# Kernel tuning notes

Measured on AMD Instinct MI355X. Metric: run time of the kernel, lower is better.

## Reference

```python
import jax, jax.numpy as jnp
import numpy as np

N_SRC = 50000
N_DST = 50000
N_EDGES = 800000
D_IN = 256
NUM_HEADS = 8
OUT_DIM = 16
NEG_SLOPE = 0.2


def setup_inputs() -> dict:
    key = jax.random.key(0)
    ks = jax.random.split(key, 9)
    feat_src = jax.random.normal(ks[0], (N_SRC, D_IN), dtype=jnp.float32)
    feat_dst = jax.random.normal(ks[1], (N_DST, D_IN), dtype=jnp.float32)
    W_src = jax.random.normal(ks[2], (NUM_HEADS * OUT_DIM, D_IN), dtype=jnp.float32) * 0.05
    b_src = jax.random.normal(ks[3], (NUM_HEADS * OUT_DIM,), dtype=jnp.float32) * 0.05
    W_dst = jax.random.normal(ks[4], (NUM_HEADS * OUT_DIM, D_IN), dtype=jnp.float32) * 0.05
    b_dst = jax.random.normal(ks[5], (NUM_HEADS * OUT_DIM,), dtype=jnp.float32) * 0.05
    attn = jax.random.normal(ks[6], (NUM_HEADS, 2 * OUT_DIM), dtype=jnp.float32) * 0.1
    src_idx = jax.random.randint(ks[7], (N_EDGES,), 0, N_SRC, dtype=jnp.int32)
    dst_idx = jax.random.randint(ks[8], (N_EDGES,), 0, N_DST, dtype=jnp.int32)
    return {"feat_src": feat_src, "feat_dst": feat_dst, "W_src": W_src,
            "b_src": b_src, "W_dst": W_dst, "b_dst": b_dst, "attn": attn,
            "src_idx": src_idx, "dst_idx": dst_idx}


def reference(feat_src, feat_dst, W_src, b_src, W_dst, b_dst, attn, src_idx, dst_idx):
    # Node-type-specific linear transforms (feat_drop=0 at inference)
    hs = (feat_src @ W_src.T + b_src).reshape(N_SRC, NUM_HEADS, OUT_DIM)
    hd = (feat_dst @ W_dst.T + b_dst).reshape(N_DST, NUM_HEADS, OUT_DIM)
    # Per-node attention logits: el_i = <hs_i, a_l>, er_j = <hd_j, a_r>
    el = jnp.einsum('nkd,kd->nk', hs, attn[:, :OUT_DIM])  # (N_src, K)
    er = jnp.einsum('nkd,kd->nk', hd, attn[:, OUT_DIM:])  # (N_dst, K)
    # Edge scores: e_uv = LeakyReLU(el_u + er_v)
    e = el[src_idx] + er[dst_idx]                          # (E, K)
    e = jnp.where(e >= 0, e, NEG_SLOPE * e)
    # Edge softmax over incoming edges of each destination node
    m = jax.ops.segment_max(e, dst_idx, num_segments=N_DST)        # (N_dst, K)
    e_exp = jnp.exp(e - m[dst_idx])
    denom = jax.ops.segment_sum(e_exp, dst_idx, num_segments=N_DST)
    a = e_exp / denom[dst_idx]                             # (E, K)
    # Weighted neighbor aggregation: sum_u a_uv * hs_u
    msg = hs[src_idx] * a[:, :, None]                      # (E, K, d_out)
    out = jax.ops.segment_sum(msg, dst_idx, num_segments=N_DST)
    return out.reshape(N_DST, NUM_HEADS * OUT_DIM)
```

## Files before the change

### kernel.cpp

```cpp
#include <hip/hip_runtime.h>
#include <hip/hip_bf16.h>

#define N_SRCC 50000
#define N_DSTC 50000
#define N_EDG 800000
#define NBUK 500
#define DPB 100
#define BCAP 2048
#define EPB 3334
#define NPB 240
#define GEMB 391

typedef __attribute__((ext_vector_type(8))) short bf16x8;
typedef __attribute__((ext_vector_type(4))) float f32x4;
typedef __attribute__((ext_vector_type(8))) unsigned short us8;

__device__ inline short f2bf(float x) {
  __hip_bfloat16 b = __float2bfloat16(x);
  return *reinterpret_cast<short*>(&b);
}
__device__ inline float bf2f(unsigned hi16) {
  union { unsigned u; float f; } c; c.u = hi16 << 16; return c.f;
}

__global__ void fold_kernel(const float* __restrict__ Wsrc, const float* __restrict__ bsrc,
                            const float* __restrict__ Wdst, const float* __restrict__ bdst,
                            const float* __restrict__ attn,
                            float* __restrict__ U, float* __restrict__ Cc,
                            short* __restrict__ Wbf, short* __restrict__ Ubf,
                            int* __restrict__ bCur) {
  int t = blockIdx.x * blockDim.x + threadIdx.x;
  if (t < 4096) {
    int side = t >> 11;
    int r = (t >> 8) & 7;
    int c = t & 255;
    const float* W = side ? Wdst : Wsrc;
    float s = 0.f;
    #pragma unroll
    for (int d = 0; d < 16; d++)
      s += attn[r*32 + side*16 + d] * W[(r*16 + d)*256 + c];
    U[t] = s;
    if (side == 1) Ubf[r*256 + c] = f2bf(s);
    else           Ubf[2048 + t]  = 0;
    const float4* p = (const float4*)&Wsrc[t*8];
    float4 v0 = p[0], v1 = p[1];
    bf16x8 w;
    w[0]=f2bf(v0.x); w[1]=f2bf(v0.y); w[2]=f2bf(v0.z); w[3]=f2bf(v0.w);
    w[4]=f2bf(v1.x); w[5]=f2bf(v1.y); w[6]=f2bf(v1.z); w[7]=f2bf(v1.w);
    *(bf16x8*)&Wbf[t*8] = w;
  }
  if (t < 16) {
    int side = t >> 3, r = t & 7;
    const float* b = side ? bdst : bsrc;
    float s = 0.f;
    #pragma unroll
    for (int d = 0; d < 16; d++) s += attn[r*32 + side*16 + d] * b[r*16 + d];
    Cc[t] = s;
  }
  if (t < NBUK) bCur[t] = 0;
}

__global__ __launch_bounds__(256) void mega(
    const float* __restrict__ feat_src, const float* __restrict__ feat_dst,
    const short* __restrict__ Wbf, const short* __restrict__ Ubf,
    const float* __restrict__ bias, const float* __restrict__ attn,
    const float* __restrict__ Cc,
    const int* __restrict__ src, const int* __restrict__ dst,
    int* __restrict__ bCur, unsigned* __restrict__ bData,
    __hip_bfloat16* __restrict__ hsC, float* __restrict__ el,
    float* __restrict__ er) {
  __shared__ __align__(16) char smem[20480];
  int b = blockIdx.x;
  int t = threadIdx.x;

  if (b < NPB) {
    int* h   = (int*)smem;
    int* cur = (int*)(smem + 2048);
    for (int i = t; i < NBUK; i += 256) h[i] = 0;
    __syncthreads();
    int start = b * EPB;
    int end = min(start + EPB, N_EDG);
    for (int e = start + t; e < end; e += 256)
      atomicAdd(&h[dst[e] / DPB], 1);
    __syncthreads();
    for (int i = t; i < NBUK; i += 256) {
      int c = h[i];
      cur[i] = c ? atomicAdd(&bCur[i], c) : 0;
    }
    __syncthreads();
    for (int e = start + t; e < end; e += 256) {
      int d = dst[e], bk = d / DPB;
      int pos = atomicAdd(&cur[bk], 1);
      if (pos < BCAP)
        bData[(size_t)bk*BCAP + pos] = (unsigned)src[e] | ((unsigned)(d - bk*DPB) << 16);
    }
    return;
  }

  if (b < NPB + GEMB) {
    short (*As)[40] = (short(*)[40])smem;
    short (*Bs)[40] = (short(*)[40])(smem + 10240);
    int lane = t & 63, wid = t >> 6;
    int wr = wid >> 1, wc = wid & 1;
    int row0 = (b - NPB) * 128;
    int lr = lane & 15, lk = lane >> 4;
    int sr = t >> 1, skq = (t & 1) * 16;
    f32x4 acc[4][4] = {};
    for (int k0 = 0; k0 < 256; k0 += 32) {
      {
        int gr = row0 + sr;
        float4 v0 = {}, v1 = {}, v2 = {}, v3 = {};
        if (gr < N_SRCC) {
          const float4* p = (const float4*)&feat_src[(size_t)gr*256 + k0 + skq];
          v0 = p[0]; v1 = p[1]; v2 = p[2]; v3 = p[3];
        }
        bf16x8 t0, t1;
        t0[0]=f2bf(v0.x); t0[1]=f2bf(v0.y); t0[2]=f2bf(v0.z); t0[3]=f2bf(v0.w);
        t0[4]=f2bf(v1.x); t0[5]=f2bf(v1.y); t0[6]=f2bf(v1.z); t0[7]=f2bf(v1.w);
        t1[0]=f2bf(v2.x); t1[1]=f2bf(v2.y); t1[2]=f2bf(v2.z); t1[3]=f2bf(v2.w);
        t1[4]=f2bf(v3.x); t1[5]=f2bf(v3.y); t1[6]=f2bf(v3.z); t1[7]=f2bf(v3.w);
        *(bf16x8*)&As[sr][skq]     = t0;
        *(bf16x8*)&As[sr][skq + 8] = t1;
      }
      *(bf16x8*)&Bs[sr][skq]     = *(const bf16x8*)&Wbf[sr*256 + k0 + skq];
      *(bf16x8*)&Bs[sr][skq + 8] = *(const bf16x8*)&Wbf[sr*256 + k0 + skq + 8];
      __syncthreads();
      bf16x8 af[4], bfr[4];
      #pragma unroll
      for (int m = 0; m < 4; m++)
        af[m] = *(const bf16x8*)&As[wr*64 + m*16 + lr][lk*8];
      #pragma unroll
      for (int n = 0; n < 4; n++)
        bfr[n] = *(const bf16x8*)&Bs[wc*64 + n*16 + lr][lk*8];
      #pragma unroll
      for (int m = 0; m < 4; m++)
        #pragma unroll
        for (int n = 0; n < 4; n++)
          acc[m][n] = __builtin_amdgcn_mfma_f32_16x16x32_bf16(af[m], bfr[n], acc[m][n], 0, 0, 0);
      __syncthreads();
    }
    #pragma unroll
    for (int m = 0; m < 4; m++) {
      int r0 = row0 + wr*64 + m*16 + lk*4;
      #pragma unroll
      for (int n = 0; n < 4; n++) {
        int col = wc*64 + n*16 + lr;
        int h = wc*4 + n;
        float bv = bias[col];
        float al = attn[h*32 + lr];
        #pragma unroll
        for (int j = 0; j < 4; j++) {
          int gr = r0 + j;
          float hv = acc[m][n][j] + bv;
          if (gr < N_SRCC) hsC[(size_t)gr*128 + col] = __float2bfloat16(hv);
          float p = hv * al;
          p += __shfl_xor(p, 1); p += __shfl_xor(p, 2);
          p += __shfl_xor(p, 4); p += __shfl_xor(p, 8);
          if (lr == 0 && gr < N_SRCC) el[gr*8 + h] = p;
        }
      }
    }
    return;
  }

  {
    short (*As)[40]  = (short(*)[40])smem;
    short (*Bu)[264] = (short(*)[264])(smem + 10240);
    int lane = t & 63, wid = t >> 6;
    int row0 = (b - NPB - GEMB) * 128;
    int lr = lane & 15, lk = lane >> 4;
    int sr = t >> 1, skq = (t & 1) * 16;
    #pragma unroll
    for (int i = 0; i < 2; i++) {
      int c = t + i*256;
      int r = c >> 5, ck = c & 31;
      *(bf16x8*)&Bu[r][ck*8] = *(const bf16x8*)&Ubf[r*256 + ck*8];
    }
    f32x4 acc[2] = {};
    for (int k0 = 0; k0 < 256; k0 += 32) {
      {
        int gr = row0 + sr;
        float4 v0 = {}, v1 = {}, v2 = {}, v3 = {};
        if (gr < N_DSTC) {
          const float4* p = (const float4*)&feat_dst[(size_t)gr*256 + k0 + skq];
          v0 = p[0]; v1 = p[1]; v2 = p[2]; v3 = p[3];
        }
        bf16x8 t0, t1;
        t0[0]=f2bf(v0.x); t0[1]=f2bf(v0.y); t0[2]=f2bf(v0.z); t0[3]=f2bf(v0.w);
        t0[4]=f2bf(v1.x); t0[5]=f2bf(v1.y); t0[6]=f2bf(v1.z); t0[7]=f2bf(v1.w);
        t1[0]=f2bf(v2.x); t1[1]=f2bf(v2.y); t1[2]=f2bf(v2.z); t1[3]=f2bf(v2.w);
        t1[4]=f2bf(v3.x); t1[5]=f2bf(v3.y); t1[6]=f2bf(v3.z); t1[7]=f2bf(v3.w);
        *(bf16x8*)&As[sr][skq]     = t0;
        *(bf16x8*)&As[sr][skq + 8] = t1;
      }
      __syncthreads();
      bf16x8 bu = *(const bf16x8*)&Bu[lr][k0 + lk*8];
      #pragma unroll
      for (int m = 0; m < 2; m++) {
        bf16x8 af = *(const bf16x8*)&As[wid*32 + m*16 + lr][lk*8];
        acc[m] = __builtin_amdgcn_mfma_f32_16x16x32_bf16(af, bu, acc[m], 0, 0, 0);
      }
      __syncthreads();
    }
    if (lr < 8) {
      float cb = Cc[8 + lr];
      #pragma unroll
      for (int m = 0; m < 2; m++) {
        int r0 = row0 + wid*32 + m*16 + lk*4;
        #pragma unroll
        for (int j = 0; j < 4; j++) {
          int gr = r0 + j;
          if (gr < N_DSTC) er[gr*8 + lr] = acc[m][j] + cb;
        }
      }
    }
  }
}

__global__ __launch_bounds__(256) void sort_bucket(const unsigned* __restrict__ bData,
    const int* __restrict__ bCur, int* __restrict__ offS, int* __restrict__ offE,
    unsigned short* __restrict__ srcS) {
  __shared__ int hist[DPB];
  __shared__ int s[128];
  __shared__ int cur[DPB];
  int b = blockIdx.x, t = threadIdx.x;
  int cnt = min(bCur[b], BCAP);
  int base = b * BCAP;
  for (int i = t; i < DPB; i += 256) hist[i] = 0;
  __syncthreads();
  for (int e = t; e < cnt; e += 256) atomicAdd(&hist[bData[base + e] >> 16], 1);
  __syncthreads();
  if (t < 128) s[t] = (t < DPB) ? hist[t] : 0;
  __syncthreads();
  for (int d = 1; d < 128; d <<= 1) {
    int v = (t < 128 && t >= d) ? s[t - d] : 0;
    __syncthreads();
    if (t < 128) s[t] += v;
    __syncthreads();
  }
  if (t < DPB) {
    int excl = s[t] - hist[t];
    cur[t] = excl;
    offS[b * DPB + t] = base + excl;
    offE[b * DPB + t] = base + excl + hist[t];
  }
  __syncthreads();
  for (int e = t; e < cnt; e += 256) {
    unsigned ent = bData[base + e];
    int pos = atomicAdd(&cur[ent >> 16], 1);
    srcS[base + pos] = (unsigned short)(ent & 0xffffu);
  }
}

__global__ __launch_bounds__(256) void aggregate(
    const __hip_bfloat16* __restrict__ hs, const float* __restrict__ el,
    const float* __restrict__ er, const int* __restrict__ offS,
    const int* __restrict__ offE, const unsigned short* __restrict__ srcS,
    float* __restrict__ out) {
  int w = threadIdx.x >> 6;
  int lane = threadIdx.x & 63;
  int jA = blockIdx.x * 8 + w;
  int jB = jA + 4;
  int g = lane >> 4;
  int q = lane & 15;
  int h = q >> 1;
  int e0a = offS[jA], remA = offE[jA] - e0a;
  int e0b = offS[jB], remB = offE[jB] - e0b;
  float erA = er[jA*8 + h];
  float erB = er[jB*8 + h];
  float accA[8] = {}, accB[8] = {};
  float denA = 0.f, denB = 0.f;

  #define AGG_BODY(E, ERH, ACC, DEN) { \
    int s = srcS[E]; \
    float ev = el[s*8 + h] + ERH; \
    ev = ev >= 0.f ? ev : 0.2f * ev; \
    float wg = __expf(ev); \
    DEN += wg; \
    us8 hv = *(const us8*)&hs[(size_t)s*128 + q*8]; \
    _Pragma("unroll") \
    for (int c = 0; c < 8; c++) { \
      ACC[c] = fmaf(wg, bf2f((unsigned)hv[c]), ACC[c]); \
    } \
  }

  int ka = 0, kb = 0;
  while (ka + 8 <= remA && kb + 8 <= remB) {
    AGG_BODY(e0a + ka + g, erA, accA, denA);
    AGG_BODY(e0b + kb + g, erB, accB, denB);
    AGG_BODY(e0a + ka + 4 + g, erA, accA, denA);
    AGG_BODY(e0b + kb + 4 + g, erB, accB, denB);
    ka += 8; kb += 8;
  }
  while (ka + 4 <= remA && kb + 4 <= remB) {
    AGG_BODY(e0a + ka + g, erA, accA, denA);
    AGG_BODY(e0b + kb + g, erB, accB, denB);
    ka += 4; kb += 4;
  }
  while (ka + 4 <= remA) { AGG_BODY(e0a + ka + g, erA, accA, denA); ka += 4; }
  while (kb + 4 <= remB) { AGG_BODY(e0b + kb + g, erB, accB, denB); kb += 4; }
  if (ka + g < remA) AGG_BODY(e0a + ka + g, erA, accA, denA);
  if (kb + g < remB) AGG_BODY(e0b + kb + g, erB, accB, denB);
  #undef AGG_BODY

  #pragma unroll
  for (int c = 0; c < 8; c++) {
    accA[c] += __shfl_xor(accA[c], 16); accA[c] += __shfl_xor(accA[c], 32);
    accB[c] += __shfl_xor(accB[c], 16); accB[c] += __shfl_xor(accB[c], 32);
  }
  denA += __shfl_xor(denA, 16); denA += __shfl_xor(denA, 32);
  denB += __shfl_xor(denB, 16); denB += __shfl_xor(denB, 32);
  if (g == 0) {
    float invA = (remA > 0) ? 1.f / denA : 0.f;
    float invB = (remB > 0) ? 1.f / denB : 0.f;
    float4 r0, r1;
    r0.x = accA[0]*invA; r0.y = accA[1]*invA; r0.z = accA[2]*invA; r0.w = accA[3]*invA;
    r1.x = accA[4]*invA; r1.y = accA[5]*invA; r1.z = accA[6]*invA; r1.w = accA[7]*invA;
    *(float4*)&out[(size_t)jA*128 + q*8]     = r0;
    *(float4*)&out[(size_t)jA*128 + q*8 + 4] = r1;
    r0.x = accB[0]*invB; r0.y = accB[1]*invB; r0.z = accB[2]*invB; r0.w = accB[3]*invB;
    r1.x = accB[4]*invB; r1.y = accB[5]*invB; r1.z = accB[6]*invB; r1.w = accB[7]*invB;
    *(float4*)&out[(size_t)jB*128 + q*8]     = r0;
    *(float4*)&out[(size_t)jB*128 + q*8 + 4] = r1;
  }
}

extern "C" void kernel_launch(void* const* d_in, const int* in_sizes, int n_in,
                              void* d_out, int out_size, void* d_ws, size_t ws_size,
                              hipStream_t stream) {
  const float* feat_src = (const float*)d_in[0];
  const float* feat_dst = (const float*)d_in[1];
  const float* W_src = (const float*)d_in[2];
  const float* b_src = (const float*)d_in[3];
  const float* W_dst = (const float*)d_in[4];
  const float* b_dst = (const float*)d_in[5];
  const float* attn  = (const float*)d_in[6];
  const int* src_idx = (const int*)d_in[7];
  const int* dst_idx = (const int*)d_in[8];
  float* out = (float*)d_out;

  __hip_bfloat16* hs_bf = (__hip_bfloat16*)d_ws;
  float* el = (float*)(hs_bf + (size_t)N_SRCC*128);
  float* er = el + (size_t)N_SRCC*8;
  float* U  = er + (size_t)N_DSTC*8;
  float* Cc = U + 4096;
  short* Wbf = (short*)(Cc + 16);
  short* Ubf = Wbf + 32768;
  int* bCur  = (int*)(Ubf + 4096);
  int* offS  = bCur + NBUK;
  int* offE  = offS + N_DSTC;
  unsigned* bData = (unsigned*)(offE + N_DSTC);
  unsigned short* srcS = (unsigned short*)(bData + (size_t)NBUK*BCAP);

  fold_kernel<<<16, 256, 0, stream>>>(W_src, b_src, W_dst, b_dst, attn, U, Cc, Wbf, Ubf, bCur);
  mega<<<NPB + 2*GEMB, 256, 0, stream>>>(feat_src, feat_dst, Wbf, Ubf, b_src, attn,
                                         Cc, src_idx, dst_idx, bCur, bData,
                                         hs_bf, el, er);
  sort_bucket<<<NBUK, 256, 0, stream>>>(bData, bCur, offS, offE, srcS);
  aggregate<<<(N_DSTC + 7)/8, 256, 0, stream>>>(hs_bf, el, er, offS, offE, srcS, out);
}
```

Baseline: 86.60 us.

## Widen fused mega kernel to 512 threads with 256-row GEMM tiles

```diff
diff --git a/kernel.cpp b/kernel.cpp
--- a/kernel.cpp
+++ b/kernel.cpp
@@ -9,7 +9,8 @@
 #define BCAP 2048
 #define EPB 3334
 #define NPB 240
-#define GEMB 391
+#define HSB 196
+#define ERB 196
 
 typedef __attribute__((ext_vector_type(8))) short bf16x8;
 typedef __attribute__((ext_vector_type(4))) float f32x4;
@@ -60,7 +61,7 @@
   if (t < NBUK) bCur[t] = 0;
 }
 
-__global__ __launch_bounds__(256) void mega(
+__global__ __launch_bounds__(512) void mega512(
     const float* __restrict__ feat_src, const float* __restrict__ feat_dst,
     const short* __restrict__ Wbf, const short* __restrict__ Ubf,
     const float* __restrict__ bias, const float* __restrict__ attn,
@@ -69,26 +70,26 @@
     int* __restrict__ bCur, unsigned* __restrict__ bData,
     __hip_bfloat16* __restrict__ hsC, float* __restrict__ el,
     float* __restrict__ er) {
-  __shared__ __align__(16) char smem[20480];
+  __shared__ __align__(16) char smem[30720];
   int b = blockIdx.x;
   int t = threadIdx.x;
 
   if (b < NPB) {
     int* h   = (int*)smem;
     int* cur = (int*)(smem + 2048);
-    for (int i = t; i < NBUK; i += 256) h[i] = 0;
+    for (int i = t; i < NBUK; i += 512) h[i] = 0;
     __syncthreads();
     int start = b * EPB;
     int end = min(start + EPB, N_EDG);
-    for (int e = start + t; e < end; e += 256)
+    for (int e = start + t; e < end; e += 512)
       atomicAdd(&h[dst[e] / DPB], 1);
     __syncthreads();
-    for (int i = t; i < NBUK; i += 256) {
+    for (int i = t; i < NBUK; i += 512) {
       int c = h[i];
       cur[i] = c ? atomicAdd(&bCur[i], c) : 0;
     }
     __syncthreads();
-    for (int e = start + t; e < end; e += 256) {
+    for (int e = start + t; e < end; e += 512) {
       int d = dst[e], bk = d / DPB;
       int pos = atomicAdd(&cur[bk], 1);
       if (pos < BCAP)
@@ -97,15 +98,17 @@
     return;
   }
 
-  if (b < NPB + GEMB) {
+  if (b < NPB + HSB) {
     short (*As)[40] = (short(*)[40])smem;
-    short (*Bs)[40] = (short(*)[40])(smem + 10240);
+    short (*Bs)[40] = (short(*)[40])(smem + 20480);
     int lane = t & 63, wid = t >> 6;
     int wr = wid >> 1, wc = wid & 1;
-    int row0 = (b - NPB) * 128;
+    int row0 = (b - NPB) * 256;
     int lr = lane & 15, lk = lane >> 4;
     int sr = t >> 1, skq = (t & 1) * 16;
+    int br = t >> 2, bq = (t & 3) * 8;
     f32x4 acc[4][4] = {};
+
     for (int k0 = 0; k0 < 256; k0 += 32) {
       {
         int gr = row0 + sr;
@@ -122,8 +125,7 @@
         *(bf16x8*)&As[sr][skq]     = t0;
         *(bf16x8*)&As[sr][skq + 8] = t1;
       }
-      *(bf16x8*)&Bs[sr][skq]     = *(const bf16x8*)&Wbf[sr*256 + k0 + skq];
-      *(bf16x8*)&Bs[sr][skq + 8] = *(const bf16x8*)&Wbf[sr*256 + k0 + skq + 8];
+      *(bf16x8*)&Bs[br][bq] = *(const bf16x8*)&Wbf[br*256 + k0 + bq];
       __syncthreads();
       bf16x8 af[4], bfr[4];
       #pragma unroll
@@ -165,15 +167,13 @@
 
   {
     short (*As)[40]  = (short(*)[40])smem;
-    short (*Bu)[264] = (short(*)[264])(smem + 10240);
-    int lane = t & 63, wid = t >> 6;
-    int row0 = (b - NPB - GEMB) * 128;
+    short (*Bu)[264] = (short(*)[264])(smem + 20480);
+    int lane = t & 63, w = t >> 6;
+    int row0 = (b - NPB - HSB) * 256;
     int lr = lane & 15, lk = lane >> 4;
     int sr = t >> 1, skq = (t & 1) * 16;
-    #pragma unroll
-    for (int i = 0; i < 2; i++) {
-      int c = t + i*256;
-      int r = c >> 5, ck = c & 31;
+    {
+      int r = t >> 5, ck = t & 31;
       *(bf16x8*)&Bu[r][ck*8] = *(const bf16x8*)&Ubf[r*256 + ck*8];
     }
     f32x4 acc[2] = {};
@@ -197,7 +197,7 @@
       bf16x8 bu = *(const bf16x8*)&Bu[lr][k0 + lk*8];
       #pragma unroll
       for (int m = 0; m < 2; m++) {
-        bf16x8 af = *(const bf16x8*)&As[wid*32 + m*16 + lr][lk*8];
+        bf16x8 af = *(const bf16x8*)&As[w*32 + m*16 + lr][lk*8];
         acc[m] = __builtin_amdgcn_mfma_f32_16x16x32_bf16(af, bu, acc[m], 0, 0, 0);
       }
       __syncthreads();
@@ -206,11 +206,11 @@
       float cb = Cc[8 + lr];
       #pragma unroll
       for (int m = 0; m < 2; m++) {
-        int r0 = row0 + wid*32 + m*16 + lk*4;
+        int r0 = row0 + w*32 + m*16 + lk*4;
         #pragma unroll
         for (int j = 0; j < 4; j++) {
-          int gr = r0 + j;
-          if (gr < N_DSTC) er[gr*8 + lr] = acc[m][j] + cb;
+          int gr2 = r0 + j;
+          if (gr2 < N_DSTC) er[gr2*8 + lr] = acc[m][j] + cb;
         }
       }
     }
@@ -353,9 +353,9 @@
   unsigned short* srcS = (unsigned short*)(bData + (size_t)NBUK*BCAP);
 
   fold_kernel<<<16, 256, 0, stream>>>(W_src, b_src, W_dst, b_dst, attn, U, Cc, Wbf, Ubf, bCur);
-  mega<<<NPB + 2*GEMB, 256, 0, stream>>>(feat_src, feat_dst, Wbf, Ubf, b_src, attn,
-                                         Cc, src_idx, dst_idx, bCur, bData,
-                                         hs_bf, el, er);
+  mega512<<<NPB + HSB + ERB, 512, 0, stream>>>(feat_src, feat_dst, Wbf, Ubf, b_src, attn,
+                                               Cc, src_idx, dst_idx, bCur, bData,
+                                               hs_bf, el, er);
   sort_bucket<<<NBUK, 256, 0, stream>>>(bData, bCur, offS, offE, srcS);
   aggregate<<<(N_DSTC + 7)/8, 256, 0, stream>>>(hs_bf, el, er, offS, offE, srcS, out);
 }
```

Measured after the change: 89.09 us. +2.9%, slower.
